# Optimization experiments

Measured on AMD Instinct MI355X. Metric: run time of the kernel, lower is better.

Reference implementation:

```python
import jax, jax.numpy as jnp
import numpy as np

EPS = 1e-9
N = 32768


def signed_area(poly):
    # poly: [..., K, 2] -> signed shoelace area (CCW positive)
    x = poly[..., 0]; y = poly[..., 1]
    x2 = jnp.roll(x, -1, axis=-1); y2 = jnp.roll(y, -1, axis=-1)
    return 0.5 * jnp.sum(x * y2 - x2 * y, axis=-1)


def convex_hull_pad(pts):
    # pts: [K,2] -> [K,2] CCW convex-hull vertices, padded by repeating the last hull vertex.
    K = pts.shape[0]
    a = pts[:, None, None, :]; b = pts[None, :, None, :]; c = pts[None, None, :, :]
    # cr[i,j,k] = cross(p_j - p_i, p_k - p_i); edge i->j on hull iff all points left of it
    cr = (b - a)[..., 0] * (c - a)[..., 1] - (b - a)[..., 1] * (c - a)[..., 0]
    not_eye = ~jnp.eye(K, dtype=bool)
    is_edge = jnp.all(cr >= -1e-7, axis=2) & not_eye
    on_hull = jnp.any(is_edge, axis=1)
    w = on_hull.astype(pts.dtype)
    cen = (pts * w[:, None]).sum(0) / jnp.maximum(w.sum(), 1.0)
    ang = jnp.arctan2(pts[:, 1] - cen[1], pts[:, 0] - cen[0])
    order = jnp.argsort(jnp.where(on_hull, ang, jnp.inf))  # hull verts first, CCW by angle
    sp = pts[order]; sv = on_hull[order]
    last = sp[jnp.maximum(on_hull.sum() - 1, 0)]
    return jnp.where(sv[:, None], sp, last[None, :])


def clip_convex(subject, clip):
    # Sutherland-Hodgman: subject [S,2] CCW polygon (trailing duplicate padding OK),
    # clip [C,2] CCW convex polygon. Fixed-size, jit-friendly.
    S = subject.shape[0]
    poly = subject
    b_all = jnp.roll(clip, -1, axis=0)
    for i in range(clip.shape[0]):  # static small loop over clip edges
        a = clip[i]; b = b_all[i]
        p = poly; q = jnp.roll(poly, -1, axis=0)
        ex = b[0] - a[0]; ey = b[1] - a[1]
        dp = ex * (p[:, 1] - a[1]) - ey * (p[:, 0] - a[0])
        dq = ex * (q[:, 1] - a[1]) - ey * (q[:, 0] - a[0])
        in_p = dp >= 0; in_q = dq >= 0
        denom = dp - dq
        t = dp / jnp.where(jnp.abs(denom) < EPS, EPS, denom)
        inter = p + t[:, None] * (q - p)
        cand = jnp.stack([inter, q], axis=1).reshape(2 * S, 2)
        flags = jnp.stack([in_p != in_q, in_q], axis=1).reshape(2 * S)
        order = jnp.argsort(1 - flags.astype(jnp.int32))  # stable: valid verts first, order kept
        cand = cand[order]; flags = flags[order]
        last = cand[jnp.maximum(flags.sum() - 1, 0)]
        poly = jnp.where(flags[:, None], cand, last[None, :])[:S]
    return poly


def giou_one(pred18, target8):
    P = pred18.reshape(9, 2)
    T = target8.reshape(4, 2)
    sa = signed_area(T)
    T_ccw = jnp.where(sa < 0, T[::-1], T)
    hullA = convex_hull_pad(P)  # [9,2]
    areaA = jnp.abs(signed_area(hullA))
    areaB = jnp.abs(sa)
    # pad subject to 16 verts (clipped 9-gon has <= 13 verts)
    subj = jnp.concatenate([hullA, jnp.broadcast_to(hullA[-1], (7, 2))], axis=0)
    inter = jnp.abs(signed_area(clip_convex(subj, T_ccw)))
    union = areaA + areaB - inter
    hullC = convex_hull_pad(jnp.concatenate([P, T], axis=0))  # enclosing hull of 13 pts
    areaC = jnp.abs(signed_area(hullC))
    return inter / jnp.maximum(union, EPS) - (areaC - union) / jnp.maximum(areaC, EPS)


def setup_inputs():
    key = jax.random.key(0)
    k1, k2, k3, k4, k5, k6 = jax.random.split(key, 6)
    # pred: 9 rep-points scattered around a random center
    ctr = jax.random.uniform(k1, (N, 1, 2), minval=0.0, maxval=1024.0)
    off = jax.random.normal(k2, (N, 9, 2)) * 24.0
    pred = (ctr + off).reshape(N, 18).astype(jnp.float32)
    # target: rotated-rectangle corners [N,8]
    tc = jax.random.uniform(k3, (N, 1, 2), minval=0.0, maxval=1024.0)
    wh = jax.random.uniform(k4, (N, 1, 2), minval=16.0, maxval=128.0)
    ang = jax.random.uniform(k5, (N, 1), minval=0.0, maxval=2.0 * np.pi)
    unit = jnp.array([[-0.5, -0.5], [0.5, -0.5], [0.5, 0.5], [-0.5, 0.5]], jnp.float32)
    xy = unit[None] * wh  # [N,4,2]
    ca = jnp.cos(ang); sn = jnp.sin(ang)
    rx = xy[..., 0] * ca - xy[..., 1] * sn
    ry = xy[..., 0] * sn + xy[..., 1] * ca
    target = (jnp.stack([rx, ry], axis=-1) + tc).reshape(N, 8).astype(jnp.float32)
    weight = jax.random.uniform(k6, (N,), dtype=jnp.float32)
    return {"pred": pred, "target": target, "weight": weight}


def reference(pred, target, weight):
    gious = jax.vmap(giou_one)(pred, target)  # [N]
    loss = (1.0 - gious) * weight
    return jnp.mean(loss)  # reduction='mean', loss_weight=1.0
```

## Files before the change

kernel.cpp:

```cpp
#include <hip/hip_runtime.h>
#include <math.h>

#define EPSD 1e-9

template<int K>
__device__ __forceinline__ void sortxy(double (&x)[K], double (&y)[K]) {
#pragma unroll
    for (int r = 0; r < K; r++) {
#pragma unroll
        for (int j = (r & 1); j + 1 < K; j += 2) {
            bool sw = (x[j] > x[j + 1]) || ((x[j] == x[j + 1]) && (y[j] > y[j + 1]));
            double tx = x[j], ty = y[j];
            x[j] = sw ? x[j + 1] : tx;
            y[j] = sw ? y[j + 1] : ty;
            x[j + 1] = sw ? tx : x[j + 1];
            y[j + 1] = sw ? ty : y[j + 1];
        }
    }
}

template<int K>
__device__ __forceinline__ int chain_hull(const double (&sx)[K], const double (&sy)[K],
                                          double2* Hb) {
    int k = 0;
    double t1x = 0.0, t1y = 0.0, t2x = 0.0, t2y = 0.0;
#define PUSH_(PX, PY)                                                         \
    {                                                                         \
        if (k >= 2) Hb[(k - 2) * 64] = make_double2(t2x, t2y);                \
        t2x = t1x; t2y = t1y; t1x = (PX); t1y = (PY); k++;                    \
    }
#define POPS_(PX, PY, LIM)                                                    \
    while (k >= (LIM) &&                                                      \
           ((t1x - t2x) * ((PY) - t2y) - (t1y - t2y) * ((PX) - t2x)) <= 0.0) {\
        k--;                                                                  \
        t1x = t2x; t1y = t2y;                                                 \
        if (k >= 2) { double2 v_ = Hb[(k - 2) * 64]; t2x = v_.x; t2y = v_.y; }\
    }
#pragma unroll
    for (int i = 0; i < K; i++) {
        double px = sx[i], py = sy[i];
        POPS_(px, py, 2);
        PUSH_(px, py);
    }
    const int lim = k + 1;
#pragma unroll
    for (int i = K - 2; i >= 0; i--) {
        double px = sx[i], py = sy[i];
        POPS_(px, py, lim);
        PUSH_(px, py);
    }
#undef PUSH_
#undef POPS_
    if (k >= 2) Hb[(k - 2) * 64] = make_double2(t2x, t2y);
    Hb[(k - 1) * 64] = make_double2(t1x, t1y);
    return k - 1;
}

__global__ __launch_bounds__(64)
void giou_kernel(const float* __restrict__ pred,
                 const float* __restrict__ target,
                 const float* __restrict__ weight,
                 double* __restrict__ ws,
                 int n) {
    __shared__ double2 Hs[16 * 64];
    double2* Hb = &Hs[threadIdx.x];
    const int lane = threadIdx.x;
    const int odd = lane & 1;
    const int i0 = blockIdx.x * 32 + (lane >> 1);
    const bool valid = i0 < n;
    const int i = valid ? i0 : (n > 0 ? n - 1 : 0);

    double Tx[4], Ty[4];
    {
        const float4* tp = (const float4*)target + (size_t)i * 2;
        float4 t0 = tp[0], t1 = tp[1];
        Tx[0] = t0.x; Ty[0] = t0.y; Tx[1] = t0.z; Ty[1] = t0.w;
        Tx[2] = t1.x; Ty[2] = t1.y; Tx[3] = t1.z; Ty[3] = t1.w;
    }
    double saT = 0.5 * ((Tx[0] * Ty[1] - Tx[1] * Ty[0]) + (Tx[1] * Ty[2] - Tx[2] * Ty[1]) +
                        (Tx[2] * Ty[3] - Tx[3] * Ty[2]) + (Tx[3] * Ty[0] - Tx[0] * Ty[3]));
    double areaB = fabs(saT);
    bool rev = saT < 0.0;
    double tcx[4], tcy[4];
#pragma unroll
    for (int k = 0; k < 4; k++) {
        tcx[k] = rev ? Tx[3 - k] : Tx[k];
        tcy[k] = rev ? Ty[3 - k] : Ty[k];
    }

    double X[13], Y[13];
    {
        const float2* pp = (const float2*)pred + (size_t)i * 9;
#pragma unroll
        for (int k = 0; k < 9; k++) { float2 v = pp[k]; X[k] = v.x; Y[k] = v.y; }
    }
#pragma unroll
    for (int k = 0; k < 4; k++) {
        X[9 + k] = odd ? Tx[k] : X[0];
        Y[9 + k] = odd ? Ty[k] : Y[0];
    }

    sortxy<13>(X, Y);
    int m = chain_hull<13>(X, Y, Hb);

    double area;
    {
        double2 h0 = Hb[0];
        double px = h0.x, py = h0.y, s = 0.0;
#pragma unroll 1
        for (int j = 1; j < m; j++) {
            double2 c = Hb[j * 64];
            s += px * c.y - c.x * py;
            px = c.x; py = c.y;
        }
        s += px * h0.y - h0.x * py;
        area = fabs(0.5 * s);
    }
    double other = __shfl_xor(area, 1, 64);
    double areaA = odd ? other : area;
    double areaC = odd ? area : other;
    int mo = __shfl_xor(m, 1, 64);
    const int mA = odd ? mo : m;
    __syncthreads();
    const double2* HA = odd ? &Hs[lane - 1] : Hb;

    double S = 0.0;
    if (!odd) {
#pragma unroll 1
        for (int j = 0; j < mA; j++) {
            double2 p = HA[j * 64];
            int j1 = (j + 1 == mA) ? 0 : j + 1;
            double2 q = HA[j1 * 64];
            double lo = 0.0, hi = 1.0;
#pragma unroll
            for (int e = 0; e < 4; e++) {
                double ax = tcx[e], ay = tcy[e];
                int e1 = (e + 1) & 3;
                double ex_ = tcx[e1] - ax, ey_ = tcy[e1] - ay;
                double s0 = ex_ * (p.y - ay) - ey_ * (p.x - ax);
                double s1 = ex_ * (q.y - ay) - ey_ * (q.x - ax);
                bool in0 = s0 >= 0.0, in1 = s1 >= 0.0;
                if (!in0 && !in1) { lo = 1.0; hi = 0.0; }
                else if (in0 != in1) {
                    double t = s0 / (s0 - s1);
                    if (!in0) lo = fmax(lo, t); else hi = fmin(hi, t);
                }
            }
            if (lo < hi) {
                double dx_ = q.x - p.x, dy_ = q.y - p.y;
                double A0x = p.x + lo * dx_, A0y = p.y + lo * dy_;
                double B0x = p.x + hi * dx_, B0y = p.y + hi * dy_;
                S += A0x * B0y - B0x * A0y;
            }
        }
    } else if (mA >= 2) {
        double lo[4] = {0.0, 0.0, 0.0, 0.0}, hi[4] = {1.0, 1.0, 1.0, 1.0};
#pragma unroll 1
        for (int j = 0; j < mA; j++) {
            double2 a = HA[j * 64];
            int j1 = (j + 1 == mA) ? 0 : j + 1;
            double2 b = HA[j1 * 64];
            double ex_ = b.x - a.x, ey_ = b.y - a.y;
#pragma unroll
            for (int k = 0; k < 4; k++) {
                int k1 = (k + 1) & 3;
                double s0 = ex_ * (tcy[k] - a.y) - ey_ * (tcx[k] - a.x);
                double s1 = ex_ * (tcy[k1] - a.y) - ey_ * (tcx[k1] - a.x);
                bool in0 = s0 >= 0.0, in1 = s1 >= 0.0;
                if (!in0 && !in1) { lo[k] = 1.0; hi[k] = 0.0; }
                else if (in0 != in1) {
                    double t = s0 / (s0 - s1);
                    if (!in0) lo[k] = fmax(lo[k], t); else hi[k] = fmin(hi[k], t);
                }
            }
        }
#pragma unroll
        for (int k = 0; k < 4; k++) {
            if (lo[k] < hi[k]) {
                int k1 = (k + 1) & 3;
                double dx_ = tcx[k1] - tcx[k], dy_ = tcy[k1] - tcy[k];
                double A0x = tcx[k] + lo[k] * dx_, A0y = tcy[k] + lo[k] * dy_;
                double B0x = tcx[k] + hi[k] * dx_, B0y = tcy[k] + hi[k] * dy_;
                S += A0x * B0y - B0x * A0y;
            }
        }
    }
    double So = __shfl_xor(S, 1, 64);
    double inter = fabs(0.5 * (S + So));

    double uni = areaA + areaB - inter;
    double giou = inter / fmax(uni, EPSD) - (areaC - uni) / fmax(areaC, EPSD);
    double loss = (1.0 - giou) * (double)weight[i];
    double contrib = (!odd && valid) ? loss : 0.0;

#pragma unroll
    for (int off = 32; off > 0; off >>= 1) contrib += __shfl_down(contrib, off, 64);
    if (lane == 0) ws[blockIdx.x] = contrib;
}

__global__ __launch_bounds__(256)
void reduce_kernel(const double* __restrict__ ws, float* __restrict__ out,
                   int nb, double invN) {
    int t = threadIdx.x;
    double s = 0.0;
    for (int j = t; j < nb; j += 256) s += ws[j];
#pragma unroll
    for (int off = 32; off > 0; off >>= 1) s += __shfl_down(s, off, 64);
    __shared__ double red[4];
    if ((t & 63) == 0) red[t >> 6] = s;
    __syncthreads();
    if (t == 0) out[0] = (float)((red[0] + red[1] + red[2] + red[3]) * invN);
}

extern "C" void kernel_launch(void* const* d_in, const int* in_sizes, int n_in,
                              void* d_out, int out_size, void* d_ws, size_t ws_size,
                              hipStream_t stream) {
    const float* pred = (const float*)d_in[0];
    const float* target = (const float*)d_in[1];
    const float* weight = (const float*)d_in[2];
    float* out = (float*)d_out;
    double* ws = (double*)d_ws;
    int n = in_sizes[2];

    int grid = (n + 31) / 32;
    giou_kernel<<<grid, 64, 0, stream>>>(pred, target, weight, ws, n);
    reduce_kernel<<<1, 256, 0, stream>>>(ws, out, grid, 1.0 / (double)n);
}
```

Measured before the change: 81.02 us.

## Replace sort+monotone-chain hull with gift wrapping and branchless clipping

Replaces the odd-even transposition sort and monotone-chain hull with a Jarvis gift-wrapping hull that writes vertices to shared memory. It also loads up to 9 hull vertices into registers and runs the intersection in both directions in every lane, fully unrolled and branchless. This drops the odd/even lane split and the final shuffle, cutting divergence and shared-memory traffic in the sort and clip phases. In exchange, each lane does twice the clipping work and the hull loop runs as many wave-wide iterations as the largest hull in the wave. Assuming at most 9 hull vertices for the prediction hull could truncate results if a hull were larger.

```diff
diff --git a/kernel.cpp b/kernel.cpp
--- a/kernel.cpp
+++ b/kernel.cpp
@@ -2,59 +2,6 @@
 #include <math.h>
 
 #define EPSD 1e-9
-
-template<int K>
-__device__ __forceinline__ void sortxy(double (&x)[K], double (&y)[K]) {
-#pragma unroll
-    for (int r = 0; r < K; r++) {
-#pragma unroll
-        for (int j = (r & 1); j + 1 < K; j += 2) {
-            bool sw = (x[j] > x[j + 1]) || ((x[j] == x[j + 1]) && (y[j] > y[j + 1]));
-            double tx = x[j], ty = y[j];
-            x[j] = sw ? x[j + 1] : tx;
-            y[j] = sw ? y[j + 1] : ty;
-            x[j + 1] = sw ? tx : x[j + 1];
-            y[j + 1] = sw ? ty : y[j + 1];
-        }
-    }
-}
-
-template<int K>
-__device__ __forceinline__ int chain_hull(const double (&sx)[K], const double (&sy)[K],
-                                          double2* Hb) {
-    int k = 0;
-    double t1x = 0.0, t1y = 0.0, t2x = 0.0, t2y = 0.0;
-#define PUSH_(PX, PY)                                                         \
-    {                                                                         \
-        if (k >= 2) Hb[(k - 2) * 64] = make_double2(t2x, t2y);                \
-        t2x = t1x; t2y = t1y; t1x = (PX); t1y = (PY); k++;                    \
-    }
-#define POPS_(PX, PY, LIM)                                                    \
-    while (k >= (LIM) &&                                                      \
-           ((t1x - t2x) * ((PY) - t2y) - (t1y - t2y) * ((PX) - t2x)) <= 0.0) {\
-        k--;                                                                  \
-        t1x = t2x; t1y = t2y;                                                 \
-        if (k >= 2) { double2 v_ = Hb[(k - 2) * 64]; t2x = v_.x; t2y = v_.y; }\
-    }
-#pragma unroll
-    for (int i = 0; i < K; i++) {
-        double px = sx[i], py = sy[i];
-        POPS_(px, py, 2);
-        PUSH_(px, py);
-    }
-    const int lim = k + 1;
-#pragma unroll
-    for (int i = K - 2; i >= 0; i--) {
-        double px = sx[i], py = sy[i];
-        POPS_(px, py, lim);
-        PUSH_(px, py);
-    }
-#undef PUSH_
-#undef POPS_
-    if (k >= 2) Hb[(k - 2) * 64] = make_double2(t2x, t2y);
-    Hb[(k - 1) * 64] = make_double2(t1x, t1y);
-    return k - 1;
-}
 
 __global__ __launch_bounds__(64)
 void giou_kernel(const float* __restrict__ pred,
@@ -62,7 +9,7 @@
                  const float* __restrict__ weight,
                  double* __restrict__ ws,
                  int n) {
-    __shared__ double2 Hs[16 * 64];
+    __shared__ double2 Hs[13 * 64];
     double2* Hb = &Hs[threadIdx.x];
     const int lane = threadIdx.x;
     const int odd = lane & 1;
@@ -100,93 +47,128 @@
         Y[9 + k] = odd ? Ty[k] : Y[0];
     }
 
-    sortxy<13>(X, Y);
-    int m = chain_hull<13>(X, Y, Hb);
-
-    double area;
-    {
-        double2 h0 = Hb[0];
-        double px = h0.x, py = h0.y, s = 0.0;
+    double sxm = X[0], sym = Y[0];
+#pragma unroll
+    for (int j = 1; j < 13; j++) {
+        bool lt = (X[j] < sxm) || ((X[j] == sxm) && (Y[j] < sym));
+        sxm = lt ? X[j] : sxm;
+        sym = lt ? Y[j] : sym;
+    }
+    double cx = sxm, cy = sym;
+    double area2 = 0.0;
+    int h = 0;
+    bool done = false;
 #pragma unroll 1
-        for (int j = 1; j < m; j++) {
-            double2 c = Hb[j * 64];
-            s += px * c.y - c.x * py;
-            px = c.x; py = c.y;
-        }
-        s += px * h0.y - h0.x * py;
-        area = fabs(0.5 * s);
-    }
-    double other = __shfl_xor(area, 1, 64);
-    double areaA = odd ? other : area;
-    double areaC = odd ? area : other;
-    int mo = __shfl_xor(m, 1, 64);
-    const int mA = odd ? mo : m;
+    for (int step = 0; step < 13; step++) {
+        if (__builtin_amdgcn_ballot_w64(!done) == 0ull) break;
+        double bx = cx, by = cy;
+        double db = 0.0;
+#pragma unroll
+        for (int j = 0; j < 13; j++) {
+            double rx = X[j] - cx, ry = Y[j] - cy;
+            double dc = rx * rx + ry * ry;
+            double ox = bx - cx, oy = by - cy;
+            double cr = ox * ry - oy * rx;
+            bool rep = (dc > 0.0) &&
+                       ((db == 0.0) || (cr < 0.0) || ((cr == 0.0) && (dc > db)));
+            bx = rep ? X[j] : bx;
+            by = rep ? Y[j] : by;
+            db = rep ? dc : db;
+        }
+        if (!done) {
+            Hb[h * 64] = make_double2(cx, cy);
+            h++;
+            area2 += cx * by - bx * cy;
+        }
+        done = done || ((bx == sxm) && (by == sym)) || ((bx == cx) && (by == cy));
+        cx = bx; cy = by;
+    }
+    double area = fabs(0.5 * area2);
+
+    double areaO = __shfl_xor(area, 1, 64);
+    double areaA = odd ? areaO : area;
+    double areaC = odd ? area : areaO;
+    int hO = __shfl_xor(h, 1, 64);
+    const int mA = odd ? hO : h;
     __syncthreads();
-    const double2* HA = odd ? &Hs[lane - 1] : Hb;
+    const double2* HA = &Hs[lane & ~1];
+    double hx[9], hy[9];
+#pragma unroll
+    for (int j = 0; j < 9; j++) {
+        double2 v = HA[j * 64];
+        hx[j] = v.x; hy[j] = v.y;
+    }
 
     double S = 0.0;
-    if (!odd) {
-#pragma unroll 1
-        for (int j = 0; j < mA; j++) {
-            double2 p = HA[j * 64];
-            int j1 = (j + 1 == mA) ? 0 : j + 1;
-            double2 q = HA[j1 * 64];
-            double lo = 0.0, hi = 1.0;
-#pragma unroll
-            for (int e = 0; e < 4; e++) {
-                double ax = tcx[e], ay = tcy[e];
-                int e1 = (e + 1) & 3;
-                double ex_ = tcx[e1] - ax, ey_ = tcy[e1] - ay;
-                double s0 = ex_ * (p.y - ay) - ey_ * (p.x - ax);
-                double s1 = ex_ * (q.y - ay) - ey_ * (q.x - ax);
-                bool in0 = s0 >= 0.0, in1 = s1 >= 0.0;
-                if (!in0 && !in1) { lo = 1.0; hi = 0.0; }
-                else if (in0 != in1) {
-                    double t = s0 / (s0 - s1);
-                    if (!in0) lo = fmax(lo, t); else hi = fmin(hi, t);
-                }
-            }
-            if (lo < hi) {
-                double dx_ = q.x - p.x, dy_ = q.y - p.y;
-                double A0x = p.x + lo * dx_, A0y = p.y + lo * dy_;
-                double B0x = p.x + hi * dx_, B0y = p.y + hi * dy_;
-                S += A0x * B0y - B0x * A0y;
-            }
-        }
-    } else if (mA >= 2) {
-        double lo[4] = {0.0, 0.0, 0.0, 0.0}, hi[4] = {1.0, 1.0, 1.0, 1.0};
-#pragma unroll 1
-        for (int j = 0; j < mA; j++) {
-            double2 a = HA[j * 64];
-            int j1 = (j + 1 == mA) ? 0 : j + 1;
-            double2 b = HA[j1 * 64];
-            double ex_ = b.x - a.x, ey_ = b.y - a.y;
-#pragma unroll
-            for (int k = 0; k < 4; k++) {
-                int k1 = (k + 1) & 3;
-                double s0 = ex_ * (tcy[k] - a.y) - ey_ * (tcx[k] - a.x);
-                double s1 = ex_ * (tcy[k1] - a.y) - ey_ * (tcx[k1] - a.x);
-                bool in0 = s0 >= 0.0, in1 = s1 >= 0.0;
-                if (!in0 && !in1) { lo[k] = 1.0; hi[k] = 0.0; }
-                else if (in0 != in1) {
-                    double t = s0 / (s0 - s1);
-                    if (!in0) lo[k] = fmax(lo[k], t); else hi[k] = fmin(hi[k], t);
-                }
-            }
-        }
+#pragma unroll
+    for (int j = 0; j < 9; j++) {
+        bool real_ = (j < mA);
+        bool wrapn = (j + 1 < mA);
+        double qx_ = wrapn ? hx[(j + 1 < 9) ? j + 1 : 0] : hx[0];
+        double qy_ = wrapn ? hy[(j + 1 < 9) ? j + 1 : 0] : hy[0];
+        double px_ = hx[j], py_ = hy[j];
+        double lo = 0.0, hi = 1.0;
+#pragma unroll
+        for (int e = 0; e < 4; e++) {
+            int e1 = (e + 1) & 3;
+            double ex_ = tcx[e1] - tcx[e], ey_ = tcy[e1] - tcy[e];
+            double s0 = ex_ * (py_ - tcy[e]) - ey_ * (px_ - tcx[e]);
+            double s1 = ex_ * (qy_ - tcy[e]) - ey_ * (qx_ - tcx[e]);
+            bool in0 = s0 >= 0.0, in1 = s1 >= 0.0;
+            double den = s0 - s1;
+            double dd = (fabs(den) < 1e-300) ? 1e-300 : den;
+            double t = s0 / dd;
+            bool crs = (in0 != in1);
+            lo = (crs && !in0) ? fmax(lo, t) : lo;
+            hi = (crs && in0)  ? fmin(hi, t) : hi;
+            bool out2 = (!in0 && !in1);
+            lo = out2 ? 1.0 : lo;
+            hi = out2 ? 0.0 : hi;
+        }
+        double dxe = qx_ - px_, dye = qy_ - py_;
+        double A0x = px_ + lo * dxe, A0y = py_ + lo * dye;
+        double B0x = px_ + hi * dxe, B0y = py_ + hi * dye;
+        double c_ = A0x * B0y - B0x * A0y;
+        S += (real_ && (lo < hi)) ? c_ : 0.0;
+    }
+
+    double loT[4] = {0.0, 0.0, 0.0, 0.0}, hiT[4] = {1.0, 1.0, 1.0, 1.0};
+#pragma unroll
+    for (int j = 0; j < 9; j++) {
+        bool pr = (j < mA);
+        bool wrapn = (j + 1 < mA);
+        double ax_ = hx[j], ay_ = hy[j];
+        double bx_ = wrapn ? hx[(j + 1 < 9) ? j + 1 : 0] : hx[0];
+        double by_ = wrapn ? hy[(j + 1 < 9) ? j + 1 : 0] : hy[0];
+        double ex_ = bx_ - ax_, ey_ = by_ - ay_;
 #pragma unroll
         for (int k = 0; k < 4; k++) {
-            if (lo[k] < hi[k]) {
-                int k1 = (k + 1) & 3;
-                double dx_ = tcx[k1] - tcx[k], dy_ = tcy[k1] - tcy[k];
-                double A0x = tcx[k] + lo[k] * dx_, A0y = tcy[k] + lo[k] * dy_;
-                double B0x = tcx[k] + hi[k] * dx_, B0y = tcy[k] + hi[k] * dy_;
-                S += A0x * B0y - B0x * A0y;
-            }
-        }
-    }
-    double So = __shfl_xor(S, 1, 64);
-    double inter = fabs(0.5 * (S + So));
+            int k1 = (k + 1) & 3;
+            double s0 = ex_ * (tcy[k] - ay_) - ey_ * (tcx[k] - ax_);
+            double s1 = ex_ * (tcy[k1] - ay_) - ey_ * (tcx[k1] - ax_);
+            bool in0 = s0 >= 0.0, in1 = s1 >= 0.0;
+            double den = s0 - s1;
+            double dd = (fabs(den) < 1e-300) ? 1e-300 : den;
+            double t = s0 / dd;
+            bool crs = (in0 != in1) && pr;
+            loT[k] = (crs && !in0) ? fmax(loT[k], t) : loT[k];
+            hiT[k] = (crs && in0)  ? fmin(hiT[k], t) : hiT[k];
+            bool out2 = (!in0 && !in1) && pr;
+            loT[k] = out2 ? 1.0 : loT[k];
+            hiT[k] = out2 ? 0.0 : hiT[k];
+        }
+    }
+    bool hullOK = (mA >= 3);
+#pragma unroll
+    for (int k = 0; k < 4; k++) {
+        int k1 = (k + 1) & 3;
+        double dxe = tcx[k1] - tcx[k], dye = tcy[k1] - tcy[k];
+        double A0x = tcx[k] + loT[k] * dxe, A0y = tcy[k] + loT[k] * dye;
+        double B0x = tcx[k] + hiT[k] * dxe, B0y = tcy[k] + hiT[k] * dye;
+        double c_ = A0x * B0y - B0x * A0y;
+        S += ((loT[k] < hiT[k]) && hullOK) ? c_ : 0.0;
+    }
+    double inter = fabs(0.5 * S);
 
     double uni = areaA + areaB - inter;
     double giou = inter / fmax(uni, EPSD) - (areaC - uni) / fmax(areaC, EPSD);
```

New measurement: 78.54 us. 3.1% less time.
